# Kernel optimization log

Measured on AMD Instinct MI355X. Metric: run time of the kernel, lower is better.

## Reference

```python
import jax, jax.numpy as jnp
import numpy as np

BATCH = 8192
N_FEATURES = 512
DEPTH = 10
N_LEAVES = 2 ** DEPTH
ATOMS = N_FEATURES + 1  # include_one=True
TAU = 1.0


def eml(a, b):
    # Assumed definition of the custom binary eml op: smooth-max / log-sum-exp.
    # eml(a, b) = log(exp(a) + exp(b)), computed stably.
    return jnp.logaddexp(a, b)


def setup_inputs() -> dict:
    key = jax.random.key(0)
    k1, k2 = jax.random.split(key)
    X = jax.random.normal(k1, (BATCH, N_FEATURES), dtype=jnp.float32)
    leaf_logits = jax.random.normal(k2, (N_LEAVES, ATOMS), dtype=jnp.float32) * 0.1
    return {"X": X, "leaf_logits": leaf_logits}


def reference(X, leaf_logits):
    batch = X.shape[0]
    # atom values: prepend constant 1 (include_one=True) -> (batch, atoms)
    atom_values = jnp.concatenate([jnp.ones((batch, 1), dtype=X.dtype), X], axis=1)
    # softmax over atoms per leaf, then mix: (batch, n_leaves)
    weights = jax.nn.softmax(leaf_logits / TAU, axis=-1)
    current = jnp.einsum('ba,la->bl', atom_values, weights)
    # binary tree reduction: log2(n_leaves) steps over strided slices
    while current.shape[-1] > 1:
        current = eml(current[..., 0::2], current[..., 1::2])
    return current.squeeze(-1)  # (batch,)
```

## Files before the change

### kernel.cpp

```cpp
#include <hip/hip_runtime.h>
#include <hip/hip_bf16.h>

#define BATCH 8192
#define NF 512
#define NL 1024
#define ATOMS 513

typedef float float4v __attribute__((ext_vector_type(4)));
typedef int int4v __attribute__((ext_vector_type(4)));
typedef long long2v __attribute__((ext_vector_type(2)));

__device__ __forceinline__ unsigned char f2fp8(float x) {
    return (unsigned char)(__builtin_amdgcn_cvt_pk_fp8_f32(x, x, 0, false) & 0xff);
}


__global__ void convert_kernel(const float* __restrict__ X,
                               unsigned char* __restrict__ Xp) {
    __shared__ unsigned char tile[16 * 512];
    int t  = threadIdx.x;
    int rt = blockIdx.x;
    const float* base = X + (size_t)rt * 16 * 512;

#pragma unroll
    for (int i = 0; i < 8; ++i) {
        float4v v = *reinterpret_cast<const float4v*>(base + (size_t)i * 1024 + t * 4);
        int w = __builtin_amdgcn_cvt_pk_fp8_f32(v[0], v[1], 0, false);
        w = __builtin_amdgcn_cvt_pk_fp8_f32(v[2], v[3], w, true);
        reinterpret_cast<int*>(tile)[i * 256 + t] = w;
    }
    __syncthreads();

    int kp = t >> 5, j = t & 31;
#pragma unroll
    for (int e = 0; e < 2; ++e) {
        int ln = 2 * j + e;
        int l16 = ln & 15, quad = ln >> 4;
        const int* s0 = reinterpret_cast<const int*>(tile + l16 * 512 + (2 * kp) * 32 + quad * 8);
        const int* s1 = reinterpret_cast<const int*>(tile + l16 * 512 + (2 * kp + 1) * 32 + quad * 8);
        int4v o = (int4v){s0[0], s0[1], s1[0], s1[1]};
        *reinterpret_cast<int4v*>(Xp + (((size_t)rt * 8 + kp) * 64 + ln) * 16) = o;
    }
}

__device__ __forceinline__ size_t wp_off(int l, int k) {
    int lt = l >> 4, l16 = l & 15;
    int ks = k >> 5, kp = ks >> 1, half = ks & 1;
    int quad = (k >> 3) & 3, byt = k & 7;
    return ((size_t)((lt * 8 + kp) * 64) + quad * 16 + l16) * 16 + half * 8 + byt;
}

__global__ void softmax_kernel(const float* __restrict__ logits,
                               unsigned char* __restrict__ Wp,
                               float* __restrict__ bias) {
    int l = blockIdx.x;
    int t = threadIdx.x;
    int wave = t >> 6, lane = t & 63;
    const float* row = logits + (size_t)l * ATOMS;
    float v0 = row[t];
    float v1 = row[t + 256];
    float v2 = (t == 0) ? row[512] : -1e30f;

    __shared__ float red[8];
    float m = fmaxf(fmaxf(v0, v1), v2);
#pragma unroll
    for (int o = 32; o > 0; o >>= 1) m = fmaxf(m, __shfl_xor(m, o, 64));
    if (lane == 0) red[wave] = m;
    __syncthreads();
    float mx = fmaxf(fmaxf(red[0], red[1]), fmaxf(red[2], red[3]));

    float e0 = __expf(v0 - mx);
    float e1 = __expf(v1 - mx);
    float e2 = (t == 0) ? __expf(v2 - mx) : 0.f;
    float s = e0 + e1 + e2;
#pragma unroll
    for (int o = 32; o > 0; o >>= 1) s += __shfl_xor(s, o, 64);
    if (lane == 0) red[4 + wave] = s;
    __syncthreads();
    float inv = 1.f / (red[4] + red[5] + red[6] + red[7]);
    float inv512 = inv * 512.f;

    if (t == 0) {
        bias[l] = e0 * inv;
        Wp[wp_off(l, 511)] = f2fp8(e2 * inv512);
    } else {
        Wp[wp_off(l, t - 1)] = f2fp8(e0 * inv512);
    }
    Wp[wp_off(l, t + 255)] = f2fp8(e1 * inv512);
}

__global__ __launch_bounds__(256, 2)
void gemm_lse_kernel(const unsigned char* __restrict__ Xp,
                     const unsigned char* __restrict__ Wp,
                     const float* __restrict__ bias,
                     float* __restrict__ partial) {
    __shared__ float sums[128];

    int tid  = threadIdx.x;
    int wave = tid >> 6;
    int lane = tid & 63;
    int quad = lane >> 4;
    int l16  = lane & 15;

    int lg  = blockIdx.x & 7;
    int rsb = blockIdx.x >> 3;

    const unsigned char* pa = Xp + (((size_t)(rsb * 8 + wave * 2) * 8) * 64 + lane) * 16;
    const unsigned char* pb = Wp + (((size_t)(lg * 8) * 8) * 64 + lane) * 16;

    float4v acc[2][8];
#pragma unroll
    for (int mt = 0; mt < 2; ++mt)
#pragma unroll
        for (int nt = 0; nt < 8; ++nt)
            acc[mt][nt] = (float4v){0.f, 0.f, 0.f, 0.f};

#pragma unroll
    for (int kp = 0; kp < 8; ++kp) {
        long2v af[2], bf[8];
#pragma unroll
        for (int mt = 0; mt < 2; ++mt)
            af[mt] = *reinterpret_cast<const long2v*>(pa + (size_t)mt * 8192 + kp * 1024);
#pragma unroll
        for (int nt = 0; nt < 8; ++nt)
            bf[nt] = *reinterpret_cast<const long2v*>(pb + (size_t)nt * 8192 + kp * 1024);

#pragma unroll
        for (int mt = 0; mt < 2; ++mt)
#pragma unroll
            for (int nt = 0; nt < 8; ++nt) {
                acc[mt][nt] = __builtin_amdgcn_mfma_f32_16x16x32_fp8_fp8(
                    af[mt][0], bf[nt][0], acc[mt][nt], 0, 0, 0);
                acc[mt][nt] = __builtin_amdgcn_mfma_f32_16x16x32_fp8_fp8(
                    af[mt][1], bf[nt][1], acc[mt][nt], 0, 0, 0);
            }
    }

    float bl[8];
#pragma unroll
    for (int nt = 0; nt < 8; ++nt)
        bl[nt] = bias[lg * 128 + nt * 16 + l16];

    const float INV512 = 0.001953125f;
    float ps[2][4];
#pragma unroll
    for (int mt = 0; mt < 2; ++mt)
#pragma unroll
        for (int r = 0; r < 4; ++r) ps[mt][r] = 0.f;

#pragma unroll
    for (int nt = 0; nt < 8; ++nt)
#pragma unroll
        for (int mt = 0; mt < 2; ++mt)
#pragma unroll
            for (int r = 0; r < 4; ++r)
                ps[mt][r] += __expf(fmaf(acc[mt][nt][r], INV512, bl[nt]));

#pragma unroll
    for (int m = 1; m < 16; m <<= 1)
#pragma unroll
        for (int mt = 0; mt < 2; ++mt)
#pragma unroll
            for (int r = 0; r < 4; ++r)
                ps[mt][r] += __shfl_xor(ps[mt][r], m, 64);

    if (l16 == 0) {
#pragma unroll
        for (int mt = 0; mt < 2; ++mt)
#pragma unroll
            for (int r = 0; r < 4; ++r)
                sums[wave * 32 + mt * 16 + quad * 4 + r] = ps[mt][r];
    }
    __syncthreads();
    if (tid < 128)
        partial[(size_t)lg * BATCH + rsb * 128 + tid] = sums[tid];
}

__global__ void combine_kernel(const float* __restrict__ partial,
                               float* __restrict__ out) {
    int i = blockIdx.x * 256 + threadIdx.x;
    float s = 0.f;
#pragma unroll
    for (int c = 0; c < 8; ++c) s += partial[(size_t)c * BATCH + i];
    out[i] = logf(s);
}

extern "C" void kernel_launch(void* const* d_in, const int* in_sizes, int n_in,
                              void* d_out, int out_size, void* d_ws, size_t ws_size,
                              hipStream_t stream) {
    const float* X      = (const float*)d_in[0];
    const float* logits = (const float*)d_in[1];
    float* out = (float*)d_out;

    char* ws = (char*)d_ws;
    unsigned char* Xp = (unsigned char*)ws;
    unsigned char* Wp = (unsigned char*)(ws + (size_t)BATCH * NF);
    float* bias = (float*)(ws + (size_t)BATCH * NF + (size_t)NL * NF);
    float* part = (float*)((char*)bias + NL * sizeof(float));

    convert_kernel<<<BATCH / 16, 256, 0, stream>>>(X, Xp);
    softmax_kernel<<<NL, 256, 0, stream>>>(logits, Wp, bias);
    gemm_lse_kernel<<<(BATCH / 128) * (NL / 128), 256, 0, stream>>>(Xp, Wp, bias, part);
    combine_kernel<<<BATCH / 256, 256, 0, stream>>>(part, out);
}
```

Measured before the change: 79.33 us.

## Merge prep kernels into one launch and stage B tile in LDS

The fp8 conversion and softmax kernels become a single launch, split by block index, which removes one kernel launch and the serialization between them. In the GEMM kernel, the block's 64KB slice of packed weights is loaded once into LDS with global_load_lds and read from there, replacing per-wave global reads of B. This cuts redundant global/L2 traffic but uses 64KB of LDS per block. That may limit occupancy below the requested 2 blocks per CU and adds a sync before compute.

```diff
diff --git a/kernel.cpp b/kernel.cpp
--- a/kernel.cpp
+++ b/kernel.cpp
@@ -14,47 +14,51 @@
     return (unsigned char)(__builtin_amdgcn_cvt_pk_fp8_f32(x, x, 0, false) & 0xff);
 }
 
-
-__global__ void convert_kernel(const float* __restrict__ X,
-                               unsigned char* __restrict__ Xp) {
-    __shared__ unsigned char tile[16 * 512];
+__device__ __forceinline__ void load_lds16(const void* g, void* ldsbase) {
+    __builtin_amdgcn_global_load_lds(
+        (const __attribute__((address_space(1))) unsigned int*)g,
+        (__attribute__((address_space(3))) unsigned int*)ldsbase,
+        16, 0, 0);
+}
+
+
+#define N_CONVERT_BLOCKS 512
+#define N_SOFTMAX_BLOCKS 1024
+
+__global__ void prep_kernel(const float* __restrict__ X,
+                            const float* __restrict__ logits,
+                            unsigned char* __restrict__ Xp,
+                            unsigned char* __restrict__ Wp,
+                            float* __restrict__ bias) {
+    int bi = blockIdx.x;
     int t  = threadIdx.x;
-    int rt = blockIdx.x;
-    const float* base = X + (size_t)rt * 16 * 512;
-
-#pragma unroll
-    for (int i = 0; i < 8; ++i) {
-        float4v v = *reinterpret_cast<const float4v*>(base + (size_t)i * 1024 + t * 4);
-        int w = __builtin_amdgcn_cvt_pk_fp8_f32(v[0], v[1], 0, false);
-        w = __builtin_amdgcn_cvt_pk_fp8_f32(v[2], v[3], w, true);
-        reinterpret_cast<int*>(tile)[i * 256 + t] = w;
-    }
-    __syncthreads();
-
-    int kp = t >> 5, j = t & 31;
-#pragma unroll
-    for (int e = 0; e < 2; ++e) {
-        int ln = 2 * j + e;
-        int l16 = ln & 15, quad = ln >> 4;
-        const int* s0 = reinterpret_cast<const int*>(tile + l16 * 512 + (2 * kp) * 32 + quad * 8);
-        const int* s1 = reinterpret_cast<const int*>(tile + l16 * 512 + (2 * kp + 1) * 32 + quad * 8);
-        int4v o = (int4v){s0[0], s0[1], s1[0], s1[1]};
-        *reinterpret_cast<int4v*>(Xp + (((size_t)rt * 8 + kp) * 64 + ln) * 16) = o;
-    }
-}
-
-__device__ __forceinline__ size_t wp_off(int l, int k) {
-    int lt = l >> 4, l16 = l & 15;
-    int ks = k >> 5, kp = ks >> 1, half = ks & 1;
-    int quad = (k >> 3) & 3, byt = k & 7;
-    return ((size_t)((lt * 8 + kp) * 64) + quad * 16 + l16) * 16 + half * 8 + byt;
-}
-
-__global__ void softmax_kernel(const float* __restrict__ logits,
-                               unsigned char* __restrict__ Wp,
-                               float* __restrict__ bias) {
-    int l = blockIdx.x;
-    int t = threadIdx.x;
+
+    if (bi < N_CONVERT_BLOCKS) {
+        __shared__ unsigned char tile[16 * 512];
+        int rt = bi;
+        const float* base = X + (size_t)rt * 16 * 512;
+#pragma unroll
+        for (int i = 0; i < 8; ++i) {
+            float4v v = *reinterpret_cast<const float4v*>(base + (size_t)i * 1024 + t * 4);
+            int w = __builtin_amdgcn_cvt_pk_fp8_f32(v[0], v[1], 0, false);
+            w = __builtin_amdgcn_cvt_pk_fp8_f32(v[2], v[3], w, true);
+            reinterpret_cast<int*>(tile)[i * 256 + t] = w;
+        }
+        __syncthreads();
+        int kp = t >> 5, j = t & 31;
+#pragma unroll
+        for (int e = 0; e < 2; ++e) {
+            int ln = 2 * j + e;
+            int l16 = ln & 15, quad = ln >> 4;
+            const int* s0 = reinterpret_cast<const int*>(tile + l16 * 512 + (2 * kp) * 32 + quad * 8);
+            const int* s1 = reinterpret_cast<const int*>(tile + l16 * 512 + (2 * kp + 1) * 32 + quad * 8);
+            int4v o = (int4v){s0[0], s0[1], s1[0], s1[1]};
+            *reinterpret_cast<int4v*>(Xp + (((size_t)rt * 8 + kp) * 64 + ln) * 16) = o;
+        }
+        return;
+    }
+
+    int l = bi - N_CONVERT_BLOCKS;
     int wave = t >> 6, lane = t & 63;
     const float* row = logits + (size_t)l * ATOMS;
     float v0 = row[t];
@@ -80,6 +84,13 @@
     float inv = 1.f / (red[4] + red[5] + red[6] + red[7]);
     float inv512 = inv * 512.f;
 
+    auto wp_off = [](int l_, int k_) -> size_t {
+        int lt = l_ >> 4, l16_ = l_ & 15;
+        int ks = k_ >> 5, kp_ = ks >> 1, half = ks & 1;
+        int quad_ = (k_ >> 3) & 3, byt = k_ & 7;
+        return ((size_t)((lt * 8 + kp_) * 64) + quad_ * 16 + l16_) * 16 + half * 8 + byt;
+    };
+
     if (t == 0) {
         bias[l] = e0 * inv;
         Wp[wp_off(l, 511)] = f2fp8(e2 * inv512);
@@ -94,6 +105,7 @@
                      const unsigned char* __restrict__ Wp,
                      const float* __restrict__ bias,
                      float* __restrict__ partial) {
+    __shared__ unsigned char Bl[64 * 1024];
     __shared__ float sums[128];
 
     int tid  = threadIdx.x;
@@ -105,8 +117,15 @@
     int lg  = blockIdx.x & 7;
     int rsb = blockIdx.x >> 3;
 
-    const unsigned char* pa = Xp + (((size_t)(rsb * 8 + wave * 2) * 8) * 64 + lane) * 16;
-    const unsigned char* pb = Wp + (((size_t)(lg * 8) * 8) * 64 + lane) * 16;
+    {
+        const unsigned char* gb = Wp + (size_t)lg * 65536 + wave * 16384 + lane * 16;
+        unsigned char* lb = Bl + wave * 16384;
+#pragma unroll
+        for (int j = 0; j < 16; ++j)
+            load_lds16(gb + j * 1024, lb + j * 1024);
+    }
+
+    const unsigned char* pa = Xp + ((size_t)(rsb * 8 + wave * 2) * 8) * 1024 + lane * 16;
 
     float4v acc[2][8];
 #pragma unroll
@@ -115,6 +134,8 @@
         for (int nt = 0; nt < 8; ++nt)
             acc[mt][nt] = (float4v){0.f, 0.f, 0.f, 0.f};
 
+    __syncthreads();
+
 #pragma unroll
     for (int kp = 0; kp < 8; ++kp) {
         long2v af[2], bf[8];
@@ -123,7 +144,7 @@
             af[mt] = *reinterpret_cast<const long2v*>(pa + (size_t)mt * 8192 + kp * 1024);
 #pragma unroll
         for (int nt = 0; nt < 8; ++nt)
-            bf[nt] = *reinterpret_cast<const long2v*>(pb + (size_t)nt * 8192 + kp * 1024);
+            bf[nt] = *reinterpret_cast<const long2v*>(Bl + (nt * 8 + kp) * 1024 + lane * 16);
 
 #pragma unroll
         for (int mt = 0; mt < 2; ++mt)
@@ -198,8 +219,7 @@
     float* bias = (float*)(ws + (size_t)BATCH * NF + (size_t)NL * NF);
     float* part = (float*)((char*)bias + NL * sizeof(float));
 
-    convert_kernel<<<BATCH / 16, 256, 0, stream>>>(X, Xp);
-    softmax_kernel<<<NL, 256, 0, stream>>>(logits, Wp, bias);
+    prep_kernel<<<N_CONVERT_BLOCKS + N_SOFTMAX_BLOCKS, 256, 0, stream>>>(X, logits, Xp, Wp, bias);
     gemm_lse_kernel<<<(BATCH / 128) * (NL / 128), 256, 0, stream>>>(Xp, Wp, bias, part);
     combine_kernel<<<BATCH / 256, 256, 0, stream>>>(part, out);
 }
```

Result: no change. 78.62 us (-0.9%).
